# Kernel optimization log

Hardware: AMD Instinct MI355X
Metric: run time of the kernel (lower is better)

Reference implementation:

```python
import jax, jax.numpy as jnp
import numpy as np

B, N, F = 8, 2048, 128
H1, H2, D1 = 32, 64, 128


def setup_inputs() -> dict:
    key = jax.random.key(0)
    ks = jax.random.split(key, 10)
    x = jax.random.normal(ks[0], (B, N, F), dtype=jnp.float32)
    a = jax.random.uniform(ks[1], (B, N, N), dtype=jnp.float32)
    # GCN layer kernels (glorot-ish scale) and biases
    W1 = jax.random.normal(ks[2], (F, H1), dtype=jnp.float32) * (1.0 / np.sqrt(F))
    b1 = jnp.zeros((H1,), dtype=jnp.float32)
    W2 = jax.random.normal(ks[3], (H1, H2), dtype=jnp.float32) * (1.0 / np.sqrt(H1))
    b2 = jnp.zeros((H2,), dtype=jnp.float32)
    # Dense classifier after flatten: input dim = N * H2
    Wd = jax.random.normal(ks[4], (N * H2, D1), dtype=jnp.float32) * (1.0 / np.sqrt(N * H2))
    bd = jnp.zeros((D1,), dtype=jnp.float32)
    Wo = jax.random.normal(ks[5], (D1, 1), dtype=jnp.float32) * (1.0 / np.sqrt(D1))
    bo = jnp.zeros((1,), dtype=jnp.float32)
    return {"x": x, "a": a, "W1": W1, "b1": b1, "W2": W2, "b2": b2,
            "Wd": Wd, "bd": bd, "Wo": Wo, "bo": bo}


def reference(x, a, W1, b1, W2, b2, Wd, bd, Wo, bo):
    # GCNConv 1: relu(A @ (X @ W1) + b1)   [B,N,F] -> [B,N,H1]
    h = jax.nn.relu(jnp.einsum('bnm,bmh->bnh', a, x @ W1) + b1)
    # GCNConv 2: relu(A @ (H @ W2) + b2)   -> [B,N,H2]
    h = jax.nn.relu(jnp.einsum('bnm,bmh->bnh', a, h @ W2) + b2)
    # Flatten -> Dense(128, relu) -> (Dropout is identity at inference) -> Dense(1, sigmoid)
    h = h.reshape(h.shape[0], -1)          # [B, N*H2]
    h = jax.nn.relu(h @ Wd + bd)           # [B, D1]
    return jax.nn.sigmoid(h @ Wo + bo)     # [B, 1]
```

## Files before the change

### kernel.cpp

```cpp
#include <hip/hip_runtime.h>
#include <math.h>

#define B_  8
#define N_  2048
#define F_  128
#define H1_ 32
#define H2_ 64
#define D1_ 128
#define KS_ 4
#define KSEG_ (N_ / KS_)

typedef unsigned short u16;
typedef unsigned int   u32;
typedef __attribute__((ext_vector_type(8))) short short8;
typedef __attribute__((ext_vector_type(4))) float f32x4;

__device__ __forceinline__ void cvt_split(const float4 a, const float4 b,
                                          short8& hi, short8& lo) {
  union { short8 s; uint4 u; } Hh, Ll;
  float e[8] = {a.x, a.y, a.z, a.w, b.x, b.y, b.z, b.w};
  u32 hw[4], lw[4];
#pragma unroll
  for (int j = 0; j < 4; ++j) {
    u32 u0 = __float_as_uint(e[2 * j]), u1 = __float_as_uint(e[2 * j + 1]);
    hw[j] = (u1 & 0xFFFF0000u) | (u0 >> 16);
    float l0 = e[2 * j] - __uint_as_float(u0 & 0xFFFF0000u);
    float l1 = e[2 * j + 1] - __uint_as_float(u1 & 0xFFFF0000u);
    lw[j] = (__float_as_uint(l1) & 0xFFFF0000u) | (__float_as_uint(l0) >> 16);
  }
  Hh.u.x = hw[0]; Hh.u.y = hw[1]; Hh.u.z = hw[2]; Hh.u.w = hw[3];
  Ll.u.x = lw[0]; Ll.u.y = lw[1]; Ll.u.z = lw[2]; Ll.u.w = lw[3];
  hi = Hh.s; lo = Ll.s;
}

template<int H, int LDST>
__device__ __forceinline__ void pack_frags(const float* s, int b, int cgbase,
                                           u16* __restrict__ oh, u16* __restrict__ ol,
                                           int tid) {
  constexpr int CGRP = H / 16;
  constexpr int PASSES = H * 8 / 256;
#pragma unroll
  for (int p = 0; p < PASSES; ++p) {
    int q = tid + p * 256;
    int h = q >> 3, nn = (q & 7) * 8;
    u32 hw[4], lw[4];
#pragma unroll
    for (int j = 0; j < 4; ++j) {
      float e0 = s[(nn + 2 * j) * LDST + h], e1 = s[(nn + 2 * j + 1) * LDST + h];
      u32 u0 = __float_as_uint(e0), u1 = __float_as_uint(e1);
      hw[j] = (u1 & 0xFFFF0000u) | (u0 >> 16);
      float l0 = e0 - __uint_as_float(u0 & 0xFFFF0000u);
      float l1 = e1 - __uint_as_float(u1 & 0xFFFF0000u);
      lw[j] = (__float_as_uint(l1) & 0xFFFF0000u) | (__float_as_uint(l0) >> 16);
    }
    int ch = h >> 4, cl = h & 15;
    int cg = cgbase + (nn >> 5);
    int lanep = ((nn >> 3) & 3) * 16 + cl;
    size_t o = ((((size_t)b * CGRP + ch) * (N_ / 32) + cg) * 64 + lanep) * 8;
    *(uint4*)(oh + o) = make_uint4(hw[0], hw[1], hw[2], hw[3]);
    *(uint4*)(ol + o) = make_uint4(lw[0], lw[1], lw[2], lw[3]);
  }
}

__global__ __launch_bounds__(256) void k_xw1cvt(const float* __restrict__ x,
                                                const float* __restrict__ W1,
                                                u16* __restrict__ oh,
                                                u16* __restrict__ ol) {
  __shared__ float xs[64][F_];
  __shared__ float w1s[F_ * H1_];
  __shared__ float s[64][H1_ + 1];
  const int b = blockIdx.y;
  const int n0 = blockIdx.x * 64;
  const int tid = threadIdx.x;
  const float* xp = x + ((size_t)b * N_ + n0) * F_;
#pragma unroll
  for (int i = 0; i < 8; ++i) {
    int q = tid + i * 256;
    int r = q >> 5, c4 = (q & 31) * 4;
    *(float4*)&xs[r][c4] = *(const float4*)(xp + (size_t)r * F_ + c4);
  }
#pragma unroll
  for (int i = 0; i < 4; ++i)
    ((float4*)w1s)[tid + i * 256] = ((const float4*)W1)[tid + i * 256];
  __syncthreads();
  const int r = tid >> 2, c0 = (tid & 3) * 8;
  float acc[8] = {};
#pragma unroll
  for (int k = 0; k < F_; ++k) {
    float xv = xs[r][k];
#pragma unroll
    for (int j = 0; j < 8; ++j)
      acc[j] = fmaf(xv, w1s[k * H1_ + c0 + j], acc[j]);
  }
#pragma unroll
  for (int j = 0; j < 8; ++j) s[r][c0 + j] = acc[j];
  __syncthreads();
  pack_frags<H1_, H1_ + 1>(&s[0][0], b, blockIdx.x * 2, oh, ol, tid);
}

__global__ __launch_bounds__(256) void k_l1fuse(const float* __restrict__ P1,
                                                const float* __restrict__ b1,
                                                const float* __restrict__ W2,
                                                u16* __restrict__ oh,
                                                u16* __restrict__ ol) {
  __shared__ float h1s[64][H1_ + 1];
  __shared__ float w2s[H1_ * H2_];
  __shared__ float hw2s[64][H2_ + 1];
  const int b = blockIdx.y;
  const int n0 = blockIdx.x * 64;
  const int tid = threadIdx.x;
  constexpr int TOT = B_ * N_ * H1_;
#pragma unroll
  for (int i = 0; i < 2; ++i) {
    int q = tid + i * 256;
    int r = q >> 3, h4 = (q & 7) * 4;
    size_t base = (((size_t)b * N_) + n0 + r) * H1_ + h4;
    float4 v0 = *(const float4*)(P1 + base);
    float4 v1 = *(const float4*)(P1 + base + TOT);
    float4 v2 = *(const float4*)(P1 + base + 2 * (size_t)TOT);
    float4 v3 = *(const float4*)(P1 + base + 3 * (size_t)TOT);
    float4 bv = *(const float4*)(b1 + h4);
    h1s[r][h4 + 0] = fmaxf(v0.x + v1.x + v2.x + v3.x + bv.x, 0.f);
    h1s[r][h4 + 1] = fmaxf(v0.y + v1.y + v2.y + v3.y + bv.y, 0.f);
    h1s[r][h4 + 2] = fmaxf(v0.z + v1.z + v2.z + v3.z + bv.z, 0.f);
    h1s[r][h4 + 3] = fmaxf(v0.w + v1.w + v2.w + v3.w + bv.w, 0.f);
  }
#pragma unroll
  for (int i = 0; i < 2; ++i)
    ((float4*)w2s)[tid + i * 256] = ((const float4*)W2)[tid + i * 256];
  __syncthreads();
  const int r = tid >> 2, c0 = (tid & 3) * 16;
  float acc[16] = {};
#pragma unroll
  for (int k = 0; k < H1_; ++k) {
    float hv = h1s[r][k];
#pragma unroll
    for (int j = 0; j < 16; ++j)
      acc[j] = fmaf(hv, w2s[k * H2_ + c0 + j], acc[j]);
  }
#pragma unroll
  for (int j = 0; j < 16; ++j) hw2s[r][c0 + j] = acc[j];
  __syncthreads();
  pack_frags<H2_, H2_ + 1>(&hw2s[0][0], b, blockIdx.x * 2, oh, ol, tid);
}

template<int H>
__global__ __launch_bounds__(256, 4) void k_agemm_mfma(const float* __restrict__ A,
                                                       const u16* __restrict__ Bph,
                                                       const u16* __restrict__ Bpl,
                                                       float* __restrict__ P) {
  constexpr int NT = H / 16;
  constexpr int BK = 64;
  constexpr int NTILE = KSEG_ / BK;
  __shared__ float at[2][64][68];

  const int batch = blockIdx.y;
  const int z = blockIdx.z;
  const int m0 = blockIdx.x * 64;
  const int tid = threadIdx.x;
  const int lane = tid & 63;
  const int wave = tid >> 6;

  const float* Ab = A + (size_t)batch * N_ * N_ + (size_t)m0 * N_ + (size_t)z * KSEG_;
  const int srow = tid >> 4, scol = tid & 15;

  const size_t cg0 = (size_t)z * (KSEG_ / 32);
  const u16* bhb = Bph + ((size_t)batch * NT) * (N_ / 32) * 512 + (size_t)lane * 8;
  const u16* blb = Bpl + ((size_t)batch * NT) * (N_ / 32) * 512 + (size_t)lane * 8;

  float4 st[4];
#pragma unroll
  for (int i = 0; i < 4; ++i)
    st[i] = *(const float4*)(Ab + (size_t)(srow + 16 * i) * N_ + scol * 4);
#pragma unroll
  for (int i = 0; i < 4; ++i)
    *(float4*)&at[0][srow + 16 * i][scol * 4] = st[i];
  __syncthreads();

  f32x4 acc[NT];
#pragma unroll
  for (int c = 0; c < NT; ++c) acc[c] = (f32x4){0.f, 0.f, 0.f, 0.f};

  for (int t = 0; t < NTILE; ++t) {
    const int kk = t * BK;
    const int buf = t & 1;
    if (t + 1 < NTILE) {
#pragma unroll
      for (int i = 0; i < 4; ++i)
        st[i] = *(const float4*)(Ab + (size_t)(srow + 16 * i) * N_ + (kk + BK) + scol * 4);
      __builtin_amdgcn_sched_barrier(0);
    }
#pragma unroll
    for (int c = 0; c < 2; ++c) {
      const float* ar = &at[buf][wave * 16 + (lane & 15)][c * 32 + (lane >> 4) * 8];
      float4 a0 = *(const float4*)ar;
      float4 a1 = *(const float4*)(ar + 4);
      short8 ahi, alo;
      cvt_split(a0, a1, ahi, alo);
      const size_t co = (cg0 + (kk >> 5) + c) * 512;
#pragma unroll
      for (int ch = 0; ch < NT; ++ch) {
        union { short8 s; uint4 u; } bh, bl;
        bh.u = *(const uint4*)(bhb + ((size_t)ch * (N_ / 32)) * 512 + co);
        bl.u = *(const uint4*)(blb + ((size_t)ch * (N_ / 32)) * 512 + co);
        acc[ch] = __builtin_amdgcn_mfma_f32_16x16x32_bf16(ahi, bh.s, acc[ch], 0, 0, 0);
        acc[ch] = __builtin_amdgcn_mfma_f32_16x16x32_bf16(ahi, bl.s, acc[ch], 0, 0, 0);
        acc[ch] = __builtin_amdgcn_mfma_f32_16x16x32_bf16(alo, bh.s, acc[ch], 0, 0, 0);
      }
    }
    if (t + 1 < NTILE) {
#pragma unroll
      for (int i = 0; i < 4; ++i)
        *(float4*)&at[buf ^ 1][srow + 16 * i][scol * 4] = st[i];
    }
    __syncthreads();
  }
  const int orow = m0 + wave * 16 + ((lane >> 4) << 2);
  float* pp = P + ((size_t)(z * B_ + batch) * N_ + orow) * H + (lane & 15);
#pragma unroll
  for (int ch = 0; ch < NT; ++ch)
#pragma unroll
    for (int j = 0; j < 4; ++j)
      pp[(size_t)j * H + ch * 16] = acc[ch][j];
}

__global__ __launch_bounds__(512) void k_densefuse(const float* __restrict__ P2,
                                                   const float* __restrict__ b2,
                                                   const float* __restrict__ Wd,
                                                   float* __restrict__ part) {
  constexpr int KC = 512;
  __shared__ float hs[B_][KC];
  __shared__ float psum[B_][D1_];
  const int kc0 = blockIdx.x * KC;
  const int n0 = blockIdx.x * 8;
  const int tid = threadIdx.x;
  constexpr size_t TOT = (size_t)B_ * N_ * H2_;
#pragma unroll
  for (int i = 0; i < 2; ++i) {
    int q = tid + i * 512;
    int b = q >> 7, k4 = (q & 127) * 4;
    int nl = k4 >> 6, h = k4 & 63;
    size_t base = (((size_t)b * N_) + n0 + nl) * H2_ + h;
    float4 v0 = *(const float4*)(P2 + base);
    float4 v1 = *(const float4*)(P2 + base + TOT);
    float4 v2 = *(const float4*)(P2 + base + 2 * TOT);
    float4 v3 = *(const float4*)(P2 + base + 3 * TOT);
    float4 bv = *(const float4*)(b2 + h);
    hs[b][k4 + 0] = fmaxf(v0.x + v1.x + v2.x + v3.x + bv.x, 0.f);
    hs[b][k4 + 1] = fmaxf(v0.y + v1.y + v2.y + v3.y + bv.y, 0.f);
    hs[b][k4 + 2] = fmaxf(v0.z + v1.z + v2.z + v3.z + bv.z, 0.f);
    hs[b][k4 + 3] = fmaxf(v0.w + v1.w + v2.w + v3.w + bv.w, 0.f);
  }
  __syncthreads();
  const int d0 = (tid & 31) * 4;
  const int b  = (tid >> 5) & 7;
  const int ks = tid >> 8;
  float a0 = 0.f, a1 = 0.f, a2 = 0.f, a3 = 0.f;
  const float* wp = Wd + ((size_t)kc0 + ks * 256) * D1_ + d0;
  const float* hp = &hs[b][ks * 256];
#pragma unroll 4
  for (int k = 0; k < 256; ++k) {
    float4 w = *(const float4*)(wp + (size_t)k * D1_);
    float h = hp[k];
    a0 = fmaf(h, w.x, a0); a1 = fmaf(h, w.y, a1);
    a2 = fmaf(h, w.z, a2); a3 = fmaf(h, w.w, a3);
  }
  if (ks == 1) {
    psum[b][d0] = a0; psum[b][d0 + 1] = a1; psum[b][d0 + 2] = a2; psum[b][d0 + 3] = a3;
  }
  __syncthreads();
  if (ks == 0) {
    float* pp = part + ((size_t)blockIdx.x * B_ + b) * D1_ + d0;
    *(float4*)pp = make_float4(a0 + psum[b][d0], a1 + psum[b][d0 + 1],
                               a2 + psum[b][d0 + 2], a3 + psum[b][d0 + 3]);
  }
}

__global__ __launch_bounds__(1024) void k_dense_final(const float* __restrict__ part,
                                                      const float* __restrict__ bd,
                                                      const float* __restrict__ Wo,
                                                      const float* __restrict__ bo,
                                                      float* __restrict__ out) {
  __shared__ float hd[B_ * D1_];
  const int tid = threadIdx.x;
  float s = 0.f;
  for (int i = 0; i < 256; ++i) s += part[(size_t)i * (B_ * D1_) + tid];
  hd[tid] = fmaxf(s + bd[tid & (D1_ - 1)], 0.f);
  __syncthreads();
  if (tid < 512) {
    int w = tid >> 6, l = tid & 63;
    float v = hd[w * D1_ + l] * Wo[l] + hd[w * D1_ + 64 + l] * Wo[64 + l];
#pragma unroll
    for (int off = 32; off; off >>= 1) v += __shfl_down(v, off, 64);
    if (l == 0) out[w] = 1.f / (1.f + expf(-(v + bo[0])));
  }
}

extern "C" void kernel_launch(void* const* d_in, const int* in_sizes, int n_in,
                              void* d_out, int out_size, void* d_ws, size_t ws_size,
                              hipStream_t stream) {
  const float* x  = (const float*)d_in[0];
  const float* a  = (const float*)d_in[1];
  const float* W1 = (const float*)d_in[2];
  const float* b1 = (const float*)d_in[3];
  const float* W2 = (const float*)d_in[4];
  const float* b2 = (const float*)d_in[5];
  const float* Wd = (const float*)d_in[6];
  const float* bd = (const float*)d_in[7];
  const float* Wo = (const float*)d_in[8];
  const float* bo = (const float*)d_in[9];
  float* out = (float*)d_out;

  float* ws    = (float*)d_ws;
  float* P     = ws;
  u16*   Bt1h  = (u16*)(ws + 4194304);
  u16*   Bt1l  = (u16*)(ws + 4456448);
  u16*   Bt2h  = (u16*)(ws + 4718592);
  u16*   Bt2l  = (u16*)(ws + 5242880);
  float* dpart = ws + 5767168;

  k_xw1cvt<<<dim3(N_ / 64, B_), 256, 0, stream>>>(x, W1, Bt1h, Bt1l);
  k_agemm_mfma<H1_><<<dim3(N_ / 64, B_, KS_), 256, 0, stream>>>(a, Bt1h, Bt1l, P);
  k_l1fuse<<<dim3(N_ / 64, B_), 256, 0, stream>>>(P, b1, W2, Bt2h, Bt2l);
  k_agemm_mfma<H2_><<<dim3(N_ / 64, B_, KS_), 256, 0, stream>>>(a, Bt2h, Bt2l, P);
  k_densefuse<<<(N_ * H2_) / 512, 512, 0, stream>>>(P, b2, Wd, dpart);
  k_dense_final<<<1, 1024, 0, stream>>>(dpart, bd, Wo, bo, out);
}
```

Measured before the change: 117.8 us.

## Drop split-bf16 emulation for single rounded bf16 MFMA, raise split-K to 8

Replaces the three-pass hi/lo bf16 split emulation of fp32 GEMM with a single bf16 MFMA per tile. A is round-to-nearest-even converted to bf16 before it is staged in LDS, and B is packed only as bf16 hi. This removes two thirds of the MFMA work, the lo-buffer loads and half the LDS footprint for A. Split-K goes from 4 to 8 and the occupancy hint from 4 to 6, so the reduce kernels now sum 8 partials. The cost is lower precision in the adjacency matmuls, which could exceed tolerance, and more partial-sum traffic.

```diff
diff --git a/kernel.cpp b/kernel.cpp
--- a/kernel.cpp
+++ b/kernel.cpp
@@ -7,7 +7,7 @@
 #define H1_ 32
 #define H2_ 64
 #define D1_ 128
-#define KS_ 4
+#define KS_ 8
 #define KSEG_ (N_ / KS_)
 
 typedef unsigned short u16;
@@ -15,57 +15,40 @@
 typedef __attribute__((ext_vector_type(8))) short short8;
 typedef __attribute__((ext_vector_type(4))) float f32x4;
 
-__device__ __forceinline__ void cvt_split(const float4 a, const float4 b,
-                                          short8& hi, short8& lo) {
-  union { short8 s; uint4 u; } Hh, Ll;
-  float e[8] = {a.x, a.y, a.z, a.w, b.x, b.y, b.z, b.w};
-  u32 hw[4], lw[4];
-#pragma unroll
-  for (int j = 0; j < 4; ++j) {
-    u32 u0 = __float_as_uint(e[2 * j]), u1 = __float_as_uint(e[2 * j + 1]);
-    hw[j] = (u1 & 0xFFFF0000u) | (u0 >> 16);
-    float l0 = e[2 * j] - __uint_as_float(u0 & 0xFFFF0000u);
-    float l1 = e[2 * j + 1] - __uint_as_float(u1 & 0xFFFF0000u);
-    lw[j] = (__float_as_uint(l1) & 0xFFFF0000u) | (__float_as_uint(l0) >> 16);
-  }
-  Hh.u.x = hw[0]; Hh.u.y = hw[1]; Hh.u.z = hw[2]; Hh.u.w = hw[3];
-  Ll.u.x = lw[0]; Ll.u.y = lw[1]; Ll.u.z = lw[2]; Ll.u.w = lw[3];
-  hi = Hh.s; lo = Ll.s;
+__device__ __forceinline__ u32 rne2(float e0, float e1) {
+  u32 u0 = __float_as_uint(e0), u1 = __float_as_uint(e1);
+  u0 = (u0 + 0x7FFFu + ((u0 >> 16) & 1u)) >> 16;
+  u1 = (u1 + 0x7FFFu + ((u1 >> 16) & 1u)) & 0xFFFF0000u;
+  return u0 | u1;
+}
+__device__ __forceinline__ uint4 rne8(const float4 a, const float4 b) {
+  return make_uint4(rne2(a.x, a.y), rne2(a.z, a.w), rne2(b.x, b.y), rne2(b.z, b.w));
 }
 
 template<int H, int LDST>
 __device__ __forceinline__ void pack_frags(const float* s, int b, int cgbase,
-                                           u16* __restrict__ oh, u16* __restrict__ ol,
-                                           int tid) {
+                                           u16* __restrict__ oh, int tid) {
   constexpr int CGRP = H / 16;
   constexpr int PASSES = H * 8 / 256;
 #pragma unroll
   for (int p = 0; p < PASSES; ++p) {
     int q = tid + p * 256;
     int h = q >> 3, nn = (q & 7) * 8;
-    u32 hw[4], lw[4];
-#pragma unroll
-    for (int j = 0; j < 4; ++j) {
-      float e0 = s[(nn + 2 * j) * LDST + h], e1 = s[(nn + 2 * j + 1) * LDST + h];
-      u32 u0 = __float_as_uint(e0), u1 = __float_as_uint(e1);
-      hw[j] = (u1 & 0xFFFF0000u) | (u0 >> 16);
-      float l0 = e0 - __uint_as_float(u0 & 0xFFFF0000u);
-      float l1 = e1 - __uint_as_float(u1 & 0xFFFF0000u);
-      lw[j] = (__float_as_uint(l1) & 0xFFFF0000u) | (__float_as_uint(l0) >> 16);
-    }
+    u32 hw[4];
+#pragma unroll
+    for (int j = 0; j < 4; ++j)
+      hw[j] = rne2(s[(nn + 2 * j) * LDST + h], s[(nn + 2 * j + 1) * LDST + h]);
     int ch = h >> 4, cl = h & 15;
     int cg = cgbase + (nn >> 5);
     int lanep = ((nn >> 3) & 3) * 16 + cl;
     size_t o = ((((size_t)b * CGRP + ch) * (N_ / 32) + cg) * 64 + lanep) * 8;
     *(uint4*)(oh + o) = make_uint4(hw[0], hw[1], hw[2], hw[3]);
-    *(uint4*)(ol + o) = make_uint4(lw[0], lw[1], lw[2], lw[3]);
   }
 }
 
 __global__ __launch_bounds__(256) void k_xw1cvt(const float* __restrict__ x,
                                                 const float* __restrict__ W1,
-                                                u16* __restrict__ oh,
-                                                u16* __restrict__ ol) {
+                                                u16* __restrict__ oh) {
   __shared__ float xs[64][F_];
   __shared__ float w1s[F_ * H1_];
   __shared__ float s[64][H1_ + 1];
@@ -95,35 +78,36 @@
 #pragma unroll
   for (int j = 0; j < 8; ++j) s[r][c0 + j] = acc[j];
   __syncthreads();
-  pack_frags<H1_, H1_ + 1>(&s[0][0], b, blockIdx.x * 2, oh, ol, tid);
+  pack_frags<H1_, H1_ + 1>(&s[0][0], b, blockIdx.x * 2, oh, tid);
 }
 
 __global__ __launch_bounds__(256) void k_l1fuse(const float* __restrict__ P1,
                                                 const float* __restrict__ b1,
                                                 const float* __restrict__ W2,
-                                                u16* __restrict__ oh,
-                                                u16* __restrict__ ol) {
+                                                u16* __restrict__ oh) {
   __shared__ float h1s[64][H1_ + 1];
   __shared__ float w2s[H1_ * H2_];
   __shared__ float hw2s[64][H2_ + 1];
   const int b = blockIdx.y;
   const int n0 = blockIdx.x * 64;
   const int tid = threadIdx.x;
-  constexpr int TOT = B_ * N_ * H1_;
+  constexpr size_t TOT = (size_t)B_ * N_ * H1_;
 #pragma unroll
   for (int i = 0; i < 2; ++i) {
     int q = tid + i * 256;
     int r = q >> 3, h4 = (q & 7) * 4;
     size_t base = (((size_t)b * N_) + n0 + r) * H1_ + h4;
-    float4 v0 = *(const float4*)(P1 + base);
-    float4 v1 = *(const float4*)(P1 + base + TOT);
-    float4 v2 = *(const float4*)(P1 + base + 2 * (size_t)TOT);
-    float4 v3 = *(const float4*)(P1 + base + 3 * (size_t)TOT);
     float4 bv = *(const float4*)(b1 + h4);
-    h1s[r][h4 + 0] = fmaxf(v0.x + v1.x + v2.x + v3.x + bv.x, 0.f);
-    h1s[r][h4 + 1] = fmaxf(v0.y + v1.y + v2.y + v3.y + bv.y, 0.f);
-    h1s[r][h4 + 2] = fmaxf(v0.z + v1.z + v2.z + v3.z + bv.z, 0.f);
-    h1s[r][h4 + 3] = fmaxf(v0.w + v1.w + v2.w + v3.w + bv.w, 0.f);
+    float a0 = bv.x, a1 = bv.y, a2 = bv.z, a3 = bv.w;
+#pragma unroll
+    for (int zz = 0; zz < KS_; ++zz) {
+      float4 v = *(const float4*)(P1 + base + (size_t)zz * TOT);
+      a0 += v.x; a1 += v.y; a2 += v.z; a3 += v.w;
+    }
+    h1s[r][h4 + 0] = fmaxf(a0, 0.f);
+    h1s[r][h4 + 1] = fmaxf(a1, 0.f);
+    h1s[r][h4 + 2] = fmaxf(a2, 0.f);
+    h1s[r][h4 + 3] = fmaxf(a3, 0.f);
   }
 #pragma unroll
   for (int i = 0; i < 2; ++i)
@@ -141,18 +125,17 @@
 #pragma unroll
   for (int j = 0; j < 16; ++j) hw2s[r][c0 + j] = acc[j];
   __syncthreads();
-  pack_frags<H2_, H2_ + 1>(&hw2s[0][0], b, blockIdx.x * 2, oh, ol, tid);
+  pack_frags<H2_, H2_ + 1>(&hw2s[0][0], b, blockIdx.x * 2, oh, tid);
 }
 
 template<int H>
-__global__ __launch_bounds__(256, 4) void k_agemm_mfma(const float* __restrict__ A,
+__global__ __launch_bounds__(256, 6) void k_agemm_mfma(const float* __restrict__ A,
                                                        const u16* __restrict__ Bph,
-                                                       const u16* __restrict__ Bpl,
                                                        float* __restrict__ P) {
   constexpr int NT = H / 16;
   constexpr int BK = 64;
   constexpr int NTILE = KSEG_ / BK;
-  __shared__ float at[2][64][68];
+  __shared__ u16 at[2][64][72];
 
   const int batch = blockIdx.y;
   const int z = blockIdx.z;
@@ -162,19 +145,17 @@
   const int wave = tid >> 6;
 
   const float* Ab = A + (size_t)batch * N_ * N_ + (size_t)m0 * N_ + (size_t)z * KSEG_;
-  const int srow = tid >> 4, scol = tid & 15;
+  const int srow = tid >> 2, sc0 = (tid & 3) * 16;
 
   const size_t cg0 = (size_t)z * (KSEG_ / 32);
   const u16* bhb = Bph + ((size_t)batch * NT) * (N_ / 32) * 512 + (size_t)lane * 8;
-  const u16* blb = Bpl + ((size_t)batch * NT) * (N_ / 32) * 512 + (size_t)lane * 8;
 
   float4 st[4];
 #pragma unroll
   for (int i = 0; i < 4; ++i)
-    st[i] = *(const float4*)(Ab + (size_t)(srow + 16 * i) * N_ + scol * 4);
-#pragma unroll
-  for (int i = 0; i < 4; ++i)
-    *(float4*)&at[0][srow + 16 * i][scol * 4] = st[i];
+    st[i] = *(const float4*)(Ab + (size_t)srow * N_ + sc0 + 4 * i);
+  *(uint4*)&at[0][srow][sc0]     = rne8(st[0], st[1]);
+  *(uint4*)&at[0][srow][sc0 + 8] = rne8(st[2], st[3]);
   __syncthreads();
 
   f32x4 acc[NT];
@@ -187,31 +168,23 @@
     if (t + 1 < NTILE) {
 #pragma unroll
       for (int i = 0; i < 4; ++i)
-        st[i] = *(const float4*)(Ab + (size_t)(srow + 16 * i) * N_ + (kk + BK) + scol * 4);
+        st[i] = *(const float4*)(Ab + (size_t)srow * N_ + (kk + BK) + sc0 + 4 * i);
       __builtin_amdgcn_sched_barrier(0);
     }
 #pragma unroll
     for (int c = 0; c < 2; ++c) {
-      const float* ar = &at[buf][wave * 16 + (lane & 15)][c * 32 + (lane >> 4) * 8];
-      float4 a0 = *(const float4*)ar;
-      float4 a1 = *(const float4*)(ar + 4);
-      short8 ahi, alo;
-      cvt_split(a0, a1, ahi, alo);
+      short8 av = *(const short8*)&at[buf][wave * 16 + (lane & 15)][c * 32 + (lane >> 4) * 8];
       const size_t co = (cg0 + (kk >> 5) + c) * 512;
 #pragma unroll
       for (int ch = 0; ch < NT; ++ch) {
-        union { short8 s; uint4 u; } bh, bl;
+        union { short8 s; uint4 u; } bh;
         bh.u = *(const uint4*)(bhb + ((size_t)ch * (N_ / 32)) * 512 + co);
-        bl.u = *(const uint4*)(blb + ((size_t)ch * (N_ / 32)) * 512 + co);
-        acc[ch] = __builtin_amdgcn_mfma_f32_16x16x32_bf16(ahi, bh.s, acc[ch], 0, 0, 0);
-        acc[ch] = __builtin_amdgcn_mfma_f32_16x16x32_bf16(ahi, bl.s, acc[ch], 0, 0, 0);
-        acc[ch] = __builtin_amdgcn_mfma_f32_16x16x32_bf16(alo, bh.s, acc[ch], 0, 0, 0);
+        acc[ch] = __builtin_amdgcn_mfma_f32_16x16x32_bf16(av, bh.s, acc[ch], 0, 0, 0);
       }
     }
     if (t + 1 < NTILE) {
-#pragma unroll
-      for (int i = 0; i < 4; ++i)
-        *(float4*)&at[buf ^ 1][srow + 16 * i][scol * 4] = st[i];
+      *(uint4*)&at[buf ^ 1][srow][sc0]     = rne8(st[0], st[1]);
+      *(uint4*)&at[buf ^ 1][srow][sc0 + 8] = rne8(st[2], st[3]);
     }
     __syncthreads();
   }
@@ -241,15 +214,17 @@
     int b = q >> 7, k4 = (q & 127) * 4;
     int nl = k4 >> 6, h = k4 & 63;
     size_t base = (((size_t)b * N_) + n0 + nl) * H2_ + h;
-    float4 v0 = *(const float4*)(P2 + base);
-    float4 v1 = *(const float4*)(P2 + base + TOT);
-    float4 v2 = *(const float4*)(P2 + base + 2 * TOT);
-    float4 v3 = *(const float4*)(P2 + base + 3 * TOT);
     float4 bv = *(const float4*)(b2 + h);
-    hs[b][k4 + 0] = fmaxf(v0.x + v1.x + v2.x + v3.x + bv.x, 0.f);
-    hs[b][k4 + 1] = fmaxf(v0.y + v1.y + v2.y + v3.y + bv.y, 0.f);
-    hs[b][k4 + 2] = fmaxf(v0.z + v1.z + v2.z + v3.z + bv.z, 0.f);
-    hs[b][k4 + 3] = fmaxf(v0.w + v1.w + v2.w + v3.w + bv.w, 0.f);
+    float a0 = bv.x, a1 = bv.y, a2 = bv.z, a3 = bv.w;
+#pragma unroll
+    for (int zz = 0; zz < KS_; ++zz) {
+      float4 v = *(const float4*)(P2 + base + (size_t)zz * TOT);
+      a0 += v.x; a1 += v.y; a2 += v.z; a3 += v.w;
+    }
+    hs[b][k4 + 0] = fmaxf(a0, 0.f);
+    hs[b][k4 + 1] = fmaxf(a1, 0.f);
+    hs[b][k4 + 2] = fmaxf(a2, 0.f);
+    hs[b][k4 + 3] = fmaxf(a3, 0.f);
   }
   __syncthreads();
   const int d0 = (tid & 31) * 4;
@@ -313,16 +288,14 @@
 
   float* ws    = (float*)d_ws;
   float* P     = ws;
-  u16*   Bt1h  = (u16*)(ws + 4194304);
-  u16*   Bt1l  = (u16*)(ws + 4456448);
-  u16*   Bt2h  = (u16*)(ws + 4718592);
-  u16*   Bt2l  = (u16*)(ws + 5242880);
-  float* dpart = ws + 5767168;
-
-  k_xw1cvt<<<dim3(N_ / 64, B_), 256, 0, stream>>>(x, W1, Bt1h, Bt1l);
-  k_agemm_mfma<H1_><<<dim3(N_ / 64, B_, KS_), 256, 0, stream>>>(a, Bt1h, Bt1l, P);
-  k_l1fuse<<<dim3(N_ / 64, B_), 256, 0, stream>>>(P, b1, W2, Bt2h, Bt2l);
-  k_agemm_mfma<H2_><<<dim3(N_ / 64, B_, KS_), 256, 0, stream>>>(a, Bt2h, Bt2l, P);
+  u16*   Bt1h  = (u16*)(ws + 8388608);
+  u16*   Bt2h  = (u16*)(ws + 8650752);
+  float* dpart = ws + 9175040;
+
+  k_xw1cvt<<<dim3(N_ / 64, B_), 256, 0, stream>>>(x, W1, Bt1h);
+  k_agemm_mfma<H1_><<<dim3(N_ / 64, B_, KS_), 256, 0, stream>>>(a, Bt1h, P);
+  k_l1fuse<<<dim3(N_ / 64, B_), 256, 0, stream>>>(P, b1, W2, Bt2h);
+  k_agemm_mfma<H2_><<<dim3(N_ / 64, B_, KS_), 256, 0, stream>>>(a, Bt2h, P);
   k_densefuse<<<(N_ * H2_) / 512, 512, 0, stream>>>(P, b2, Wd, dpart);
   k_dense_final<<<1, 1024, 0, stream>>>(dpart, bd, Wo, bo, out);
 }
```

Result: faster. 113.6 us (-3.5%).
